# Optimization experiments

Measured on AMD Instinct MI355X. Metric: run time of the kernel, lower is better.

Reference implementation:

```python
import jax, jax.numpy as jnp
import numpy as np

N, LP, LD, D, H, GS = 16, 2048, 512, 256, 8, 4
HD = D // H           # head_size = 32
TAU = 1.0             # softmax_tau
ITERS = 4             # sinkhorn_iters
INF = 1.0e6


def setup_inputs() -> dict:
    key = jax.random.key(0)
    ks = jax.random.split(key, 10)
    inp = {
        "protein": jax.random.normal(ks[0], (N, LP, D), jnp.float32),
        "drug": jax.random.normal(ks[1], (N, LD, D), jnp.float32),
        "mask_prot": jax.random.bernoulli(ks[2], 0.9, (N, LP)),
        "mask_drug": jax.random.bernoulli(ks[3], 0.9, (N, LD)),
    }
    names = ["Wq_p", "Wk_p", "Wv_p", "Wq_d", "Wk_d", "Wv_d"]
    for i, name in enumerate(names):
        inp[name] = jax.random.normal(ks[4 + i], (D, D), jnp.float32) * (1.0 / np.sqrt(D))
    return inp


def _group(x, mask):
    n, L, d = x.shape
    g = L // GS
    xg = x.reshape(n, g, GS, d).mean(2)          # [N,G,D]
    mg = mask.reshape(n, g, GS).any(2)           # [N,G]
    return xg, mg


def _alpha_logits(logits, mask_row, mask_col):
    # logits: [N,L1,L2,H]; sinkhorn normalization as in the torch module
    n, L1, L2, h = logits.shape
    logits = logits * (1.0 / np.sqrt(HD))
    pair = mask_row[:, :, None, None] & mask_col[:, None, :, None]  # [N,L1,L2,1]
    logits = jnp.where(pair, logits, logits - INF)
    A = jax.nn.softmax((logits / TAU).reshape(n, L1 * L2, h), axis=1).reshape(n, L1, L2, h)
    valid = pair.astype(A.dtype)
    A = A * valid + 1e-12 * valid
    for _ in range(ITERS):
        row_sum = (A * valid).sum(2, keepdims=True) + 1e-12
        A = A / row_sum * valid
        col_sum = (A * valid).sum(1, keepdims=True) + 1e-12
        A = A / col_sum * valid
    return A * valid


def _proj(x, W):
    n, g, d = x.shape
    return (x @ W.T).reshape(n, g, H, HD)


def reference(protein, drug, mask_prot, mask_drug, Wq_p, Wk_p, Wv_p, Wq_d, Wk_d, Wv_d):
    pg, mp = _group(protein, mask_prot)   # [N,Gp,D], [N,Gp]
    dg, md = _group(drug, mask_drug)      # [N,Gd,D], [N,Gd]

    qp, kp, vp = _proj(pg, Wq_p), _proj(pg, Wk_p), _proj(pg, Wv_p)
    qd, kd, vd = _proj(dg, Wq_d), _proj(dg, Wk_d), _proj(dg, Wv_d)

    att = lambda q, k: jnp.einsum('blhd,bkhd->blkh', q, k)
    a_pp = _alpha_logits(att(qp, kp), mp, mp)
    a_pd = _alpha_logits(att(qp, kd), mp, md)
    a_dp = _alpha_logits(att(qd, kp), md, mp)
    a_dd = _alpha_logits(att(qd, kd), md, md)

    mix = lambda a, v: jnp.einsum('blkh,bkhd->blhd', a, v).reshape(a.shape[0], a.shape[1], D)
    prot_embedding = (mix(a_pp, vp) + mix(a_pd, vd)) * 0.5  # [N,Gp,D]
    drug_embedding = (mix(a_dp, vp) + mix(a_dd, vd)) * 0.5  # [N,Gd,D]

    # agg_mode == 'mean': masked mean over valid groups
    mpf = mp[..., None].astype(prot_embedding.dtype)
    mdf = md[..., None].astype(drug_embedding.dtype)
    prot_embed = (prot_embedding * mpf).sum(1) / mpf.sum(1)
    drug_embed = (drug_embedding * mdf).sum(1) / mdf.sum(1)

    query_embed = jnp.concatenate([prot_embed, drug_embed], axis=1)  # [N,2D]
    return query_embed, a_dp
```

## Files before the change

### kernel.cpp

```cpp
#include <hip/hip_runtime.h>
#include <hip/hip_bf16.h>

#define NB   16
#define DT   256
#define HT   8
#define HDT  32
#define GP   512
#define GD   128
#define SCL  0.17677669529663687f

using bf16x8 = __attribute__((ext_vector_type(8))) short;
using f32x4  = __attribute__((ext_vector_type(4))) float;

__device__ __forceinline__ short f2bf(float f) {
  __hip_bfloat16 h = __float2bfloat16(f);
  short s; __builtin_memcpy(&s, &h, 2);
  return s;
}

__device__ __forceinline__ bf16x8 cvt8(float4 a, float4 b) {
  bf16x8 r;
  r[0] = f2bf(a.x); r[1] = f2bf(a.y); r[2] = f2bf(a.z); r[3] = f2bf(a.w);
  r[4] = f2bf(b.x); r[5] = f2bf(b.y); r[6] = f2bf(b.z); r[7] = f2bf(b.w);
  return r;
}

extern "C" __global__ __launch_bounds__(256)
void k_fused_proj(const float* __restrict__ protein, const float* __restrict__ drug,
                  const int* __restrict__ mprot, const int* __restrict__ mdrug,
                  const float* __restrict__ Wk, const float* __restrict__ Wq,
                  short* __restrict__ kp_bf, short* __restrict__ qd_bf,
                  int* __restrict__ mp_g, int* __restrict__ md_g,
                  float* __restrict__ part, int* __restrict__ cntp) {
  int b = blockIdx.x, t = threadIdx.x;
  int w = t >> 6, lane = t & 63, c15 = lane & 15, g = lane >> 4;
  const float *src, *W; const int* msk; short* o; int* mg;
  int bb;
  if (b < 128) { bb = b;      src = protein; msk = mprot; W = Wk; o = kp_bf; mg = mp_g; }
  else         { bb = b - 128; src = drug;   msk = mdrug; W = Wq; o = qd_bf; mg = md_g; }
  int flatrow0 = bb * 64;

  __shared__ int gm_s[64];
  __shared__ float part_s[256];
  part_s[t] = 0.f;
  if (t < 64) {
    const int* m = msk + (size_t)(flatrow0 + t) * 4;
    int v = (m[0] | m[1] | m[2] | m[3]) ? 1 : 0;
    gm_s[t] = v;
    mg[flatrow0 + t] = v;
  }
  __syncthreads();
  if (t == 0) {
    int c = 0;
    #pragma unroll
    for (int i = 0; i < 64; ++i) c += gm_s[i];
    cntp[b] = c;
  }

  int grow = flatrow0 + w * 16 + c15;
  const float* ap = src + (size_t)grow * 1024;
  int msel = gm_s[w * 16 + c15];

  f32x4 acc[16];
  #pragma unroll
  for (int i = 0; i < 16; ++i) acc[i] = (f32x4){0.f, 0.f, 0.f, 0.f};

  #pragma unroll
  for (int ks = 0; ks < 8; ++ks) {
    int k0 = ks * 32 + g * 8;
    float4 s0  = *(const float4*)(ap + k0);
    float4 s0b = *(const float4*)(ap + k0 + 4);
    float4 s1  = *(const float4*)(ap + 256 + k0);
    float4 s1b = *(const float4*)(ap + 256 + k0 + 4);
    float4 s2  = *(const float4*)(ap + 512 + k0);
    float4 s2b = *(const float4*)(ap + 512 + k0 + 4);
    float4 s3  = *(const float4*)(ap + 768 + k0);
    float4 s3b = *(const float4*)(ap + 768 + k0 + 4);
    float4 av, bv;
    av.x = 0.25f * (s0.x + s1.x + s2.x + s3.x);
    av.y = 0.25f * (s0.y + s1.y + s2.y + s3.y);
    av.z = 0.25f * (s0.z + s1.z + s2.z + s3.z);
    av.w = 0.25f * (s0.w + s1.w + s2.w + s3.w);
    bv.x = 0.25f * (s0b.x + s1b.x + s2b.x + s3b.x);
    bv.y = 0.25f * (s0b.y + s1b.y + s2b.y + s3b.y);
    bv.z = 0.25f * (s0b.z + s1b.z + s2b.z + s3b.z);
    bv.w = 0.25f * (s0b.w + s1b.w + s2b.w + s3b.w);
    bf16x8 af = cvt8(av, bv);

    float vs[8];
    vs[0] = msel ? av.x : 0.f; vs[1] = msel ? av.y : 0.f;
    vs[2] = msel ? av.z : 0.f; vs[3] = msel ? av.w : 0.f;
    vs[4] = msel ? bv.x : 0.f; vs[5] = msel ? bv.y : 0.f;
    vs[6] = msel ? bv.z : 0.f; vs[7] = msel ? bv.w : 0.f;
    #pragma unroll
    for (int j = 0; j < 8; ++j) {
      #pragma unroll
      for (int m = 1; m <= 8; m <<= 1) vs[j] += __shfl_xor(vs[j], m, 64);
    }
    if (c15 == 0) {
      #pragma unroll
      for (int j = 0; j < 8; ++j) atomicAdd(&part_s[k0 + j], vs[j]);
    }

    #pragma unroll
    for (int ct = 0; ct < 16; ++ct) {
      const float* wp = W + (size_t)(ct * 16 + c15) * 256 + k0;
      bf16x8 bfr = cvt8(*(const float4*)wp, *(const float4*)(wp + 4));
      acc[ct] = __builtin_amdgcn_mfma_f32_16x16x32_bf16(af, bfr, acc[ct], 0, 0, 0);
    }
  }
  #pragma unroll
  for (int ct = 0; ct < 16; ++ct) {
    #pragma unroll
    for (int r = 0; r < 4; ++r) {
      o[(size_t)(flatrow0 + w * 16 + 4 * g + r) * 256 + ct * 16 + c15] = f2bf(acc[ct][r]);
    }
  }
  __syncthreads();
  part[(size_t)b * 256 + t] = part_s[t];
}

#define FOR16(X) X(0) X(1) X(2) X(3) X(4) X(5) X(6) X(7) X(8) X(9) X(10) X(11) X(12) X(13) X(14) X(15)

extern "C" __global__ __launch_bounds__(1024)
void k_scalars(const short* __restrict__ qd, const short* __restrict__ kp,
               const int* __restrict__ md_g, const int* __restrict__ mp_g,
               float* __restrict__ rcz) {
  int bid = blockIdx.x;
  int n = ((bid & 7) << 1) | ((bid >> 3) & 1);
  int h = bid >> 4;
  int tid = threadIdx.x;
  int wid = tid >> 6, lane = tid & 63;
  int wr = wid >> 1, ch = wid & 1;
  int c15 = lane & 15, g = lane >> 4;

  __shared__ float c_s[GP];
  __shared__ float r_s[GD];
  __shared__ float t_s[GD];
  __shared__ float t2[2][GD];
  __shared__ float red[8][GP];
  __shared__ float z_sh, sr_sh, sc_sh, kv_sh;
  __shared__ int mp_sh[GP];
  __shared__ int md_sh[GD];

  if (tid < GP) { int m = mp_g[n * GP + tid]; mp_sh[tid] = m; c_s[tid] = m ? 1.f : 0.f; }
  if (tid < GD) { int m = md_g[n * GD + tid]; md_sh[tid] = m; r_s[tid] = m ? 1.f : 0.f; }
  __syncthreads();

  if (wid == 0) {
    float v = (float)(mp_sh[lane] + mp_sh[lane + 64] + mp_sh[lane + 128] + mp_sh[lane + 192] +
                      mp_sh[lane + 256] + mp_sh[lane + 320] + mp_sh[lane + 384] + mp_sh[lane + 448]);
    #pragma unroll
    for (int m = 1; m <= 32; m <<= 1) v += __shfl_xor(v, m, 64);
    if (lane == 0) kv_sh = v;
  }

  int qrow = 16 * wr + c15;
  bf16x8 af = *(const bf16x8*)(qd + ((size_t)(n * GD + qrow)) * 256 + h * HDT + g * 8);
  int row0 = 16 * wr + 4 * g;
  int mr0 = md_sh[row0], mr1 = md_sh[row0 + 1], mr2 = md_sh[row0 + 2], mr3 = md_sh[row0 + 3];
  const short* kbase = kp + ((size_t)n * GP) * 256 + h * HDT + g * 8;
  int colbase = ch * 256 + c15;

#define DECLP(i) f32x4 P##i;
  FOR16(DECLP)
#define MKP(i) { int col = colbase + 16 * (i); \
    bf16x8 bfr = *(const bf16x8*)(kbase + (size_t)col * 256); \
    f32x4 a = __builtin_amdgcn_mfma_f32_16x16x32_bf16(af, bfr, (f32x4){0.f,0.f,0.f,0.f}, 0, 0, 0); \
    int mc = mp_sh[col]; \
    P##i[0] = (mc && mr0) ? __expf(a[0] * SCL) : 0.f; \
    P##i[1] = (mc && mr1) ? __expf(a[1] * SCL) : 0.f; \
    P##i[2] = (mc && mr2) ? __expf(a[2] * SCL) : 0.f; \
    P##i[3] = (mc && mr3) ? __expf(a[3] * SCL) : 0.f; }
  FOR16(MKP)

  {
    float pa0 = 0.f, pa1 = 0.f, pa2 = 0.f, pa3 = 0.f;
#define RS0(i) pa0 += P##i[0]; pa1 += P##i[1]; pa2 += P##i[2]; pa3 += P##i[3];
    FOR16(RS0)
    #pragma unroll
    for (int m = 1; m <= 8; m <<= 1) {
      pa0 += __shfl_xor(pa0, m, 64); pa1 += __shfl_xor(pa1, m, 64);
      pa2 += __shfl_xor(pa2, m, 64); pa3 += __shfl_xor(pa3, m, 64);
    }
    if (c15 == 0) t2[ch][row0 + 0] = pa0;
    if (c15 == 1) t2[ch][row0 + 1] = pa1;
    if (c15 == 2) t2[ch][row0 + 2] = pa2;
    if (c15 == 3) t2[ch][row0 + 3] = pa3;
  }
  __syncthreads();
  if (tid < GD) t_s[tid] = t2[0][tid] + t2[1][tid];
  __syncthreads();
  if (wid == 0) {
    float v = t_s[lane] + t_s[lane + 64];
    #pragma unroll
    for (int m = 1; m <= 32; m <<= 1) v += __shfl_xor(v, m, 64);
    if (lane == 0) z_sh = v;
  }
  __syncthreads();
  float Zinv = 1.0f / z_sh;
  float Sc = kv_sh;

  #pragma unroll 1
  for (int it = 0; it < 4; ++it) {
    if (tid < GD) {
      float ti = t_s[tid] * Zinv + 1e-12f * Sc;
      float ri = r_s[tid];
      r_s[tid] = md_sh[tid] ? (ri / (ri * ti + 1e-12f)) : 0.f;
    }
    __syncthreads();
    if (wid == 0) {
      float v = r_s[lane] + r_s[lane + 64];
      #pragma unroll
      for (int m = 1; m <= 32; m <<= 1) v += __shfl_xor(v, m, 64);
      if (lane == 0) sr_sh = v;
    }
    __syncthreads();
    float Sr = sr_sh;
    {
      float rr0 = r_s[row0], rr1 = r_s[row0 + 1], rr2 = r_s[row0 + 2], rr3 = r_s[row0 + 3];
#define CP(i) { float u = P##i[0] * rr0 + P##i[1] * rr1 + P##i[2] * rr2 + P##i[3] * rr3; \
      u += __shfl_xor(u, 16, 64); u += __shfl_xor(u, 32, 64); \
      if (g == 0) red[wr][colbase + 16 * (i)] = u; }
      FOR16(CP)
    }
    __syncthreads();
    if (tid < GP) {
      float cs = red[0][tid] + red[1][tid] + red[2][tid] + red[3][tid] +
                 red[4][tid] + red[5][tid] + red[6][tid] + red[7][tid];
      float uj = cs * Zinv + 1e-12f * Sr;
      float cj = c_s[tid];
      c_s[tid] = mp_sh[tid] ? (cj / (cj * uj + 1e-12f)) : 0.f;
    }
    __syncthreads();
    if (wid == 0) {
      float v = c_s[lane] + c_s[lane + 64] + c_s[lane + 128] + c_s[lane + 192] +
                c_s[lane + 256] + c_s[lane + 320] + c_s[lane + 384] + c_s[lane + 448];
      #pragma unroll
      for (int m = 1; m <= 32; m <<= 1) v += __shfl_xor(v, m, 64);
      if (lane == 0) sc_sh = v;
    }
    __syncthreads();
    Sc = sc_sh;
    if (it < 3) {
      float qa0 = 0.f, qa1 = 0.f, qa2 = 0.f, qa3 = 0.f;
#define RP(i) { float cv = c_s[colbase + 16 * (i)]; \
      qa0 += P##i[0] * cv; qa1 += P##i[1] * cv; qa2 += P##i[2] * cv; qa3 += P##i[3] * cv; }
      FOR16(RP)
      #pragma unroll
      for (int m = 1; m <= 8; m <<= 1) {
        qa0 += __shfl_xor(qa0, m, 64); qa1 += __shfl_xor(qa1, m, 64);
        qa2 += __shfl_xor(qa2, m, 64); qa3 += __shfl_xor(qa3, m, 64);
      }
      if (c15 == 0) t2[ch][row0 + 0] = qa0;
      if (c15 == 1) t2[ch][row0 + 1] = qa1;
      if (c15 == 2) t2[ch][row0 + 2] = qa2;
      if (c15 == 3) t2[ch][row0 + 3] = qa3;
      __syncthreads();
      if (tid < GD) t_s[tid] = t2[0][tid] + t2[1][tid];
    }
  }

  size_t rb = (size_t)(n * 8 + h) * 1024;
  if (tid < GD) rcz[rb + tid] = r_s[tid];
  if (tid < GP) rcz[rb + 128 + tid] = c_s[tid];
  if (tid == 0) rcz[rb + 640] = Zinv;
}

extern "C" __global__ __launch_bounds__(256)
void k_write_embed(const short* __restrict__ qd, const short* __restrict__ kp,
                   const float* __restrict__ rcz,
                   const float* __restrict__ part, const int* __restrict__ cntp,
                   const float* __restrict__ Wvp, const float* __restrict__ Wvd,
                   float* __restrict__ out) {
  int bid = blockIdx.x;
  int t = threadIdx.x;
  if (bid >= 512) {
    int bb = bid - 512;
    int n = bb >> 3;
    int dchunk = (bb & 7) * 32;
    __shared__ float sps[256], sds[256];
    float a1 = 0.f;
    #pragma unroll
    for (int i = 0; i < 8; ++i) a1 += part[(size_t)(n * 8 + i) * 256 + t];
    sps[t] = a1;
    float a2 = 0.f;
    #pragma unroll
    for (int i = 0; i < 2; ++i) a2 += part[(size_t)(128 + n * 2 + i) * 256 + t];
    sds[t] = a2;
    __syncthreads();
    int cp = 0, cd = 0;
    #pragma unroll
    for (int i = 0; i < 8; ++i) cp += cntp[n * 8 + i];
    #pragma unroll
    for (int i = 0; i < 2; ++i) cd += cntp[128 + n * 2 + i];
    int dloc = t >> 3, ks = (t & 7) * 32;
    int d = dchunk + dloc;
    const float* wp = Wvp + (size_t)d * 256 + ks;
    const float* wd = Wvd + (size_t)d * 256 + ks;
    float acc = 0.f;
    #pragma unroll
    for (int k = 0; k < 32; k += 4) {
      float4 a = *(const float4*)(wp + k);
      float4 c = *(const float4*)(wd + k);
      acc += sps[ks + k] * a.x + sps[ks + k + 1] * a.y + sps[ks + k + 2] * a.z + sps[ks + k + 3] * a.w
           + sds[ks + k] * c.x + sds[ks + k + 1] * c.y + sds[ks + k + 2] * c.z + sds[ks + k + 3] * c.w;
    }
    #pragma unroll
    for (int m = 1; m <= 4; m <<= 1) acc += __shfl_xor(acc, m, 64);
    if ((t & 7) == 0) {
      acc *= 0.5f;
      out[n * 512 + d]       = acc / (float)cp;
      out[n * 512 + 256 + d] = acc / (float)cd;
    }
    return;
  }
  int n = ((bid & 7) << 1) | ((bid >> 3) & 1);
  int rest = bid >> 4;
  int rt = rest >> 2;
  int cc = rest & 3;
  int w = t >> 6, lane = t & 63;
  int c15 = lane & 15, g = lane >> 4;

  const short* qbase = qd + ((size_t)(n * GD + rt * 16 + c15)) * 256;
  bf16x8 af[8];
  #pragma unroll
  for (int h = 0; h < 8; ++h) af[h] = *(const bf16x8*)(qbase + h * HDT + g * 8);

  size_t rb = (size_t)n * 8 * 1024;
  float rv[8][4], zin[8];
  #pragma unroll
  for (int h = 0; h < 8; ++h) {
    const float* rp = rcz + rb + (size_t)h * 1024;
    #pragma unroll
    for (int r = 0; r < 4; ++r) rv[h][r] = rp[rt * 16 + 4 * g + r];
    zin[h] = rp[640];
  }

  #pragma unroll
  for (int ct = 0; ct < 2; ++ct) {
    int col = cc * 128 + w * 32 + ct * 16 + c15;
    f32x4 acc[8]; float cw[8];
    #pragma unroll
    for (int h = 0; h < 8; ++h) {
      bf16x8 bfr = *(const bf16x8*)(kp + ((size_t)(n * GP + col)) * 256 + h * HDT + g * 8);
      acc[h] = __builtin_amdgcn_mfma_f32_16x16x32_bf16(af[h], bfr, (f32x4){0.f,0.f,0.f,0.f}, 0, 0, 0);
      cw[h] = rcz[rb + (size_t)h * 1024 + 128 + col];
    }
    #pragma unroll
    for (int r = 0; r < 4; ++r) {
      int row = rt * 16 + 4 * g + r;
      float4 lo, hi;
      lo.x = rv[0][r] * (__expf(acc[0][r] * SCL) * zin[0] + 1e-12f) * cw[0];
      lo.y = rv[1][r] * (__expf(acc[1][r] * SCL) * zin[1] + 1e-12f) * cw[1];
      lo.z = rv[2][r] * (__expf(acc[2][r] * SCL) * zin[2] + 1e-12f) * cw[2];
      lo.w = rv[3][r] * (__expf(acc[3][r] * SCL) * zin[3] + 1e-12f) * cw[3];
      hi.x = rv[4][r] * (__expf(acc[4][r] * SCL) * zin[4] + 1e-12f) * cw[4];
      hi.y = rv[5][r] * (__expf(acc[5][r] * SCL) * zin[5] + 1e-12f) * cw[5];
      hi.z = rv[6][r] * (__expf(acc[6][r] * SCL) * zin[6] + 1e-12f) * cw[6];
      hi.w = rv[7][r] * (__expf(acc[7][r] * SCL) * zin[7] + 1e-12f) * cw[7];
      float* dst = out + 8192 + (((size_t)(n * GD + row)) * GP + col) * 8;
      *(float4*)dst = lo;
      *(float4*)(dst + 4) = hi;
    }
  }
}

extern "C" void kernel_launch(void* const* d_in, const int* in_sizes, int n_in,
                              void* d_out, int out_size, void* d_ws, size_t ws_size,
                              hipStream_t stream) {
  const float* protein = (const float*)d_in[0];
  const float* drug    = (const float*)d_in[1];
  const int*   mprot   = (const int*)d_in[2];
  const int*   mdrug   = (const int*)d_in[3];
  const float* Wk_p = (const float*)d_in[5];
  const float* Wv_p = (const float*)d_in[6];
  const float* Wq_d = (const float*)d_in[7];
  const float* Wv_d = (const float*)d_in[9];
  float* out = (float*)d_out;

  char* wsb = (char*)d_ws;
  short* kp_bf = (short*)wsb;                 wsb += (size_t)NB * GP * 256 * 2;
  short* qd_bf = (short*)wsb;                 wsb += (size_t)NB * GD * 256 * 2;
  float* part  = (float*)wsb;                 wsb += (size_t)160 * 256 * 4;
  float* rcz   = (float*)wsb;                 wsb += (size_t)128 * 1024 * 4;
  int*   cntp  = (int*)wsb;                   wsb += 160 * 4;
  int*   mp_g  = (int*)wsb;                   wsb += 8192 * 4;
  int*   md_g  = (int*)wsb;                   wsb += 2048 * 4;

  k_fused_proj<<<160, 256, 0, stream>>>(protein, drug, mprot, mdrug, Wk_p, Wq_d,
                                        kp_bf, qd_bf, mp_g, md_g, part, cntp);
  k_scalars<<<128, 1024, 0, stream>>>(qd_bf, kp_bf, md_g, mp_g, rcz);
  k_write_embed<<<640, 256, 0, stream>>>(qd_bf, kp_bf, rcz, part, cntp,
                                         Wv_p, Wv_d, out);
}
```

Baseline: 186.5 us.

## Split group-mean and projection into separate kernels with bf16 weight pre-conversion

The fused grouping-plus-projection kernel (160 blocks) becomes two kernels. The first spreads the streaming group-mean reduction over 640 blocks, writes bf16 grouped activations, and converts the Wk/Wq weights to bf16 once. The second kernel runs the MFMA projection over 320 blocks, reading bf16 inputs directly. The aim is more parallelism for the bandwidth-bound input read (about 42 MB) and no repeated fp32-to-bf16 weight conversion. The cost is an extra kernel launch and a round trip of the intermediates through global memory, and the partial-sum count grows from 160 to 640.

```diff
diff --git a/kernel.cpp b/kernel.cpp
--- a/kernel.cpp
+++ b/kernel.cpp
@@ -10,6 +10,7 @@
 #define SCL  0.17677669529663687f
 
 using bf16x8 = __attribute__((ext_vector_type(8))) short;
+using bf16x4 = __attribute__((ext_vector_type(4))) short;
 using f32x4  = __attribute__((ext_vector_type(4))) float;
 
 __device__ __forceinline__ short f2bf(float f) {
@@ -26,98 +27,101 @@
 }
 
 extern "C" __global__ __launch_bounds__(256)
-void k_fused_proj(const float* __restrict__ protein, const float* __restrict__ drug,
-                  const int* __restrict__ mprot, const int* __restrict__ mdrug,
-                  const float* __restrict__ Wk, const float* __restrict__ Wq,
-                  short* __restrict__ kp_bf, short* __restrict__ qd_bf,
-                  int* __restrict__ mp_g, int* __restrict__ md_g,
-                  float* __restrict__ part, int* __restrict__ cntp) {
+void k_group(const float* __restrict__ protein, const float* __restrict__ drug,
+             const int* __restrict__ mprot, const int* __restrict__ mdrug,
+             const float* __restrict__ Wk, const float* __restrict__ Wq,
+             short* __restrict__ pg_bf, short* __restrict__ dg_bf,
+             int* __restrict__ mp_g, int* __restrict__ md_g,
+             short* __restrict__ Wk_bf, short* __restrict__ Wq_bf,
+             float* __restrict__ part, int* __restrict__ cntp) {
+  int b = blockIdx.x, t = threadIdx.x;
+  if (b >= 640) {
+    int idx = (b - 640) * 2048 + t * 8;
+    const float* s; short* d;
+    if (idx < 65536) { s = Wk + idx; d = Wk_bf + idx; }
+    else             { s = Wq + (idx - 65536); d = Wq_bf + (idx - 65536); }
+    *(bf16x8*)d = cvt8(*(const float4*)s, *(const float4*)(s + 4));
+    return;
+  }
+  const float* src; const int* msk; short* dst; int* mg; int gbase;
+  if (b < 512) { src = protein; msk = mprot; dst = pg_bf; mg = mp_g; gbase = b * 16; }
+  else         { src = drug;    msk = mdrug; dst = dg_bf; mg = md_g; gbase = (b - 512) * 16; }
+
+  __shared__ int gm_s[16];
+  __shared__ float part_s[4][256];
+  if (t < 16) {
+    const int* m = msk + (size_t)(gbase + t) * 4;
+    int v = (m[0] | m[1] | m[2] | m[3]) ? 1 : 0;
+    gm_s[t] = v;
+    mg[gbase + t] = v;
+  }
+  __syncthreads();
+  if (t == 0) {
+    int c = 0;
+    #pragma unroll
+    for (int i = 0; i < 16; ++i) c += gm_s[i];
+    cntp[b] = c;
+  }
+
+  int col4 = t & 63, gsub = t >> 6;
+  float a0 = 0.f, a1 = 0.f, a2 = 0.f, a3 = 0.f;
+  #pragma unroll
+  for (int it = 0; it < 4; ++it) {
+    int grp = gbase + gsub + it * 4;
+    const float* rp = src + (size_t)grp * 1024 + col4 * 4;
+    float4 r0 = *(const float4*)rp;
+    float4 r1 = *(const float4*)(rp + 256);
+    float4 r2 = *(const float4*)(rp + 512);
+    float4 r3 = *(const float4*)(rp + 768);
+    float m0 = 0.25f * (r0.x + r1.x + r2.x + r3.x);
+    float m1 = 0.25f * (r0.y + r1.y + r2.y + r3.y);
+    float m2 = 0.25f * (r0.z + r1.z + r2.z + r3.z);
+    float m3 = 0.25f * (r0.w + r1.w + r2.w + r3.w);
+    bf16x4 v; v[0] = f2bf(m0); v[1] = f2bf(m1); v[2] = f2bf(m2); v[3] = f2bf(m3);
+    *(bf16x4*)(dst + (size_t)grp * 256 + col4 * 4) = v;
+    if (gm_s[gsub + it * 4]) { a0 += m0; a1 += m1; a2 += m2; a3 += m3; }
+  }
+  part_s[gsub][col4 * 4 + 0] = a0;
+  part_s[gsub][col4 * 4 + 1] = a1;
+  part_s[gsub][col4 * 4 + 2] = a2;
+  part_s[gsub][col4 * 4 + 3] = a3;
+  __syncthreads();
+  part[(size_t)b * 256 + t] = part_s[0][t] + part_s[1][t] + part_s[2][t] + part_s[3][t];
+}
+
+extern "C" __global__ __launch_bounds__(256)
+void k_projbf(const short* __restrict__ pg_bf, const short* __restrict__ dg_bf,
+              const short* __restrict__ Wk_bf, const short* __restrict__ Wq_bf,
+              short* __restrict__ kp_bf, short* __restrict__ qd_bf) {
   int b = blockIdx.x, t = threadIdx.x;
   int w = t >> 6, lane = t & 63, c15 = lane & 15, g = lane >> 4;
-  const float *src, *W; const int* msk; short* o; int* mg;
-  int bb;
-  if (b < 128) { bb = b;      src = protein; msk = mprot; W = Wk; o = kp_bf; mg = mp_g; }
-  else         { bb = b - 128; src = drug;   msk = mdrug; W = Wq; o = qd_bf; mg = md_g; }
-  int flatrow0 = bb * 64;
-
-  __shared__ int gm_s[64];
-  __shared__ float part_s[256];
-  part_s[t] = 0.f;
-  if (t < 64) {
-    const int* m = msk + (size_t)(flatrow0 + t) * 4;
-    int v = (m[0] | m[1] | m[2] | m[3]) ? 1 : 0;
-    gm_s[t] = v;
-    mg[flatrow0 + t] = v;
-  }
-  __syncthreads();
-  if (t == 0) {
-    int c = 0;
-    #pragma unroll
-    for (int i = 0; i < 64; ++i) c += gm_s[i];
-    cntp[b] = c;
-  }
-
-  int grow = flatrow0 + w * 16 + c15;
-  const float* ap = src + (size_t)grow * 1024;
-  int msel = gm_s[w * 16 + c15];
-
-  f32x4 acc[16];
-  #pragma unroll
-  for (int i = 0; i < 16; ++i) acc[i] = (f32x4){0.f, 0.f, 0.f, 0.f};
+  const short *A, *W; short* o; int rowbase;
+  if (b < 256) { A = pg_bf; W = Wk_bf; o = kp_bf; rowbase = b * 32; }
+  else         { A = dg_bf; W = Wq_bf; o = qd_bf; rowbase = (b - 256) * 32; }
+  int rt = rowbase + (w & 1) * 16;
+  int ch = (w >> 1) * 128;
+
+  const short* ap = A + (size_t)(rt + c15) * 256;
+  f32x4 acc[8];
+  #pragma unroll
+  for (int i = 0; i < 8; ++i) acc[i] = (f32x4){0.f, 0.f, 0.f, 0.f};
 
   #pragma unroll
   for (int ks = 0; ks < 8; ++ks) {
-    int k0 = ks * 32 + g * 8;
-    float4 s0  = *(const float4*)(ap + k0);
-    float4 s0b = *(const float4*)(ap + k0 + 4);
-    float4 s1  = *(const float4*)(ap + 256 + k0);
-    float4 s1b = *(const float4*)(ap + 256 + k0 + 4);
-    float4 s2  = *(const float4*)(ap + 512 + k0);
-    float4 s2b = *(const float4*)(ap + 512 + k0 + 4);
-    float4 s3  = *(const float4*)(ap + 768 + k0);
-    float4 s3b = *(const float4*)(ap + 768 + k0 + 4);
-    float4 av, bv;
-    av.x = 0.25f * (s0.x + s1.x + s2.x + s3.x);
-    av.y = 0.25f * (s0.y + s1.y + s2.y + s3.y);
-    av.z = 0.25f * (s0.z + s1.z + s2.z + s3.z);
-    av.w = 0.25f * (s0.w + s1.w + s2.w + s3.w);
-    bv.x = 0.25f * (s0b.x + s1b.x + s2b.x + s3b.x);
-    bv.y = 0.25f * (s0b.y + s1b.y + s2b.y + s3b.y);
-    bv.z = 0.25f * (s0b.z + s1b.z + s2b.z + s3b.z);
-    bv.w = 0.25f * (s0b.w + s1b.w + s2b.w + s3b.w);
-    bf16x8 af = cvt8(av, bv);
-
-    float vs[8];
-    vs[0] = msel ? av.x : 0.f; vs[1] = msel ? av.y : 0.f;
-    vs[2] = msel ? av.z : 0.f; vs[3] = msel ? av.w : 0.f;
-    vs[4] = msel ? bv.x : 0.f; vs[5] = msel ? bv.y : 0.f;
-    vs[6] = msel ? bv.z : 0.f; vs[7] = msel ? bv.w : 0.f;
-    #pragma unroll
-    for (int j = 0; j < 8; ++j) {
-      #pragma unroll
-      for (int m = 1; m <= 8; m <<= 1) vs[j] += __shfl_xor(vs[j], m, 64);
-    }
-    if (c15 == 0) {
-      #pragma unroll
-      for (int j = 0; j < 8; ++j) atomicAdd(&part_s[k0 + j], vs[j]);
-    }
-
-    #pragma unroll
-    for (int ct = 0; ct < 16; ++ct) {
-      const float* wp = W + (size_t)(ct * 16 + c15) * 256 + k0;
-      bf16x8 bfr = cvt8(*(const float4*)wp, *(const float4*)(wp + 4));
+    bf16x8 af = *(const bf16x8*)(ap + ks * 32 + g * 8);
+    #pragma unroll
+    for (int ct = 0; ct < 8; ++ct) {
+      bf16x8 bfr = *(const bf16x8*)(W + (size_t)(ch + ct * 16 + c15) * 256 + ks * 32 + g * 8);
       acc[ct] = __builtin_amdgcn_mfma_f32_16x16x32_bf16(af, bfr, acc[ct], 0, 0, 0);
     }
   }
   #pragma unroll
-  for (int ct = 0; ct < 16; ++ct) {
+  for (int ct = 0; ct < 8; ++ct) {
     #pragma unroll
     for (int r = 0; r < 4; ++r) {
-      o[(size_t)(flatrow0 + w * 16 + 4 * g + r) * 256 + ct * 16 + c15] = f2bf(acc[ct][r]);
-    }
-  }
-  __syncthreads();
-  part[(size_t)b * 256 + t] = part_s[t];
+      o[(size_t)(rt + 4 * g + r) * 256 + ch + ct * 16 + c15] = f2bf(acc[ct][r]);
+    }
+  }
 }
 
 #define FOR16(X) X(0) X(1) X(2) X(3) X(4) X(5) X(6) X(7) X(8) X(9) X(10) X(11) X(12) X(13) X(14) X(15)
@@ -282,18 +286,18 @@
     __shared__ float sps[256], sds[256];
     float a1 = 0.f;
     #pragma unroll
-    for (int i = 0; i < 8; ++i) a1 += part[(size_t)(n * 8 + i) * 256 + t];
+    for (int i = 0; i < 32; ++i) a1 += part[(size_t)(n * 32 + i) * 256 + t];
     sps[t] = a1;
     float a2 = 0.f;
     #pragma unroll
-    for (int i = 0; i < 2; ++i) a2 += part[(size_t)(128 + n * 2 + i) * 256 + t];
+    for (int i = 0; i < 8; ++i) a2 += part[(size_t)(512 + n * 8 + i) * 256 + t];
     sds[t] = a2;
     __syncthreads();
     int cp = 0, cd = 0;
     #pragma unroll
-    for (int i = 0; i < 8; ++i) cp += cntp[n * 8 + i];
-    #pragma unroll
-    for (int i = 0; i < 2; ++i) cd += cntp[128 + n * 2 + i];
+    for (int i = 0; i < 32; ++i) cp += cntp[n * 32 + i];
+    #pragma unroll
+    for (int i = 0; i < 8; ++i) cd += cntp[512 + n * 8 + i];
     int dloc = t >> 3, ks = (t & 7) * 32;
     int d = dchunk + dloc;
     const float* wp = Wvp + (size_t)d * 256 + ks;
@@ -380,16 +384,22 @@
   float* out = (float*)d_out;
 
   char* wsb = (char*)d_ws;
+  short* pg_bf = (short*)wsb;                 wsb += (size_t)NB * GP * 256 * 2;
+  short* dg_bf = (short*)wsb;                 wsb += (size_t)NB * GD * 256 * 2;
   short* kp_bf = (short*)wsb;                 wsb += (size_t)NB * GP * 256 * 2;
   short* qd_bf = (short*)wsb;                 wsb += (size_t)NB * GD * 256 * 2;
-  float* part  = (float*)wsb;                 wsb += (size_t)160 * 256 * 4;
+  short* Wk_bf = (short*)wsb;                 wsb += 65536 * 2;
+  short* Wq_bf = (short*)wsb;                 wsb += 65536 * 2;
+  float* part  = (float*)wsb;                 wsb += (size_t)640 * 256 * 4;
   float* rcz   = (float*)wsb;                 wsb += (size_t)128 * 1024 * 4;
-  int*   cntp  = (int*)wsb;                   wsb += 160 * 4;
+  int*   cntp  = (int*)wsb;                   wsb += 640 * 4;
   int*   mp_g  = (int*)wsb;                   wsb += 8192 * 4;
   int*   md_g  = (int*)wsb;                   wsb += 2048 * 4;
 
-  k_fused_proj<<<160, 256, 0, stream>>>(protein, drug, mprot, mdrug, Wk_p, Wq_d,
-                                        kp_bf, qd_bf, mp_g, md_g, part, cntp);
+  k_group<<<704, 256, 0, stream>>>(protein, drug, mprot, mdrug, Wk_p, Wq_d,
+                                   pg_bf, dg_bf, mp_g, md_g, Wk_bf, Wq_bf,
+                                   part, cntp);
+  k_projbf<<<320, 256, 0, stream>>>(pg_bf, dg_bf, Wk_bf, Wq_bf, kp_bf, qd_bf);
   k_scalars<<<128, 1024, 0, stream>>>(qd_bf, kp_bf, md_g, mp_g, rcz);
   k_write_embed<<<640, 256, 0, stream>>>(qd_bf, kp_bf, rcz, part, cntp,
                                          Wv_p, Wv_d, out);
```

New measurement: 163.1 us. -12.5%, faster.
